# Optimization experiments

Measured on AMD Instinct MI355X. Metric: run time of the kernel, lower is better.

Reference implementation:

```python
import jax, jax.numpy as jnp
import numpy as np
from jax import lax

SELECTION_SIZE = 2  # top-k experts per token


def setup_inputs() -> dict:
    key = jax.random.key(0)
    k1, k2, k3, k4 = jax.random.split(key, 4)
    N, E, IN, OUT = 8192, 8, 2048, 2048
    X = jax.random.normal(k1, (N, IN), dtype=jnp.float32)
    G = jax.random.normal(k2, (N, E), dtype=jnp.float32)
    # expert Linear params: y = x @ W_e.T + b_e, W_e: [out, in]
    W = jax.random.normal(k3, (E, OUT, IN), dtype=jnp.float32) * (1.0 / np.sqrt(IN))
    b = jax.random.normal(k4, (E, OUT), dtype=jnp.float32) * 0.01
    return {"X": X, "G": G, "W": W, "b": b}


def reference(X, G, W, b):
    # softmax gating over experts, then top-k selection and renormalization
    raw_weights = jax.nn.softmax(G, axis=1)                      # [N, E]
    top_w, top_idx = lax.top_k(raw_weights, SELECTION_SIZE)      # [N, k]
    norm_w = top_w / jnp.sum(top_w, axis=1, keepdims=True)       # [N, k]

    # dense all-expert GEMM (same math as per-expert gathered matmuls)
    all_Y = jnp.einsum('ni,eoi->neo', X, W) + b[None, :, :]      # [N, E, out]

    # gather the top-k experts' outputs per token and combine
    sel_Y = jnp.take_along_axis(all_Y, top_idx[:, :, None], axis=1)  # [N, k, out]
    Y = jnp.einsum('nk,nko->no', norm_w, sel_Y)                  # [N, out]
    return Y
```

## Files before the change

kernel.cpp:

```cpp
#include <hip/hip_runtime.h>
#include <hip/hip_bf16.h>

#define N_TOK 8192
#define N_EXP 8
#define DIM_IN 2048
#define DIM_OUT 2048

#define BM 256
#define BN 256
#define BK 64
#define NKT (DIM_IN / BK)

#define NX_ELEMS (N_TOK * DIM_IN)
#define NW_ELEMS (N_EXP * DIM_OUT * DIM_IN)

typedef __attribute__((ext_vector_type(8))) short bf16x8_t;
typedef __attribute__((ext_vector_type(8))) short s16x8_t;
typedef __attribute__((ext_vector_type(4))) short s16x4_t;
typedef __attribute__((ext_vector_type(4))) float f32x4_t;

__device__ __forceinline__ short f2bf(float f) {
    union { __hip_bfloat16 h; short s; } u;
    u.h = __float2bfloat16(f);
    return u.s;
}

__device__ __forceinline__ void gload_lds16(const void* g, void* l) {
    __builtin_amdgcn_global_load_lds(
        (const __attribute__((address_space(1))) void*)g,
        (__attribute__((address_space(3))) void*)l, 16, 0, 0);
}

__global__ void moe_zero_kernel(float4* __restrict__ y, int n4, int* __restrict__ counts) {
    int i = blockIdx.x * blockDim.x + threadIdx.x;
    if (i < N_EXP) counts[i] = 0;
    float4 z; z.x = 0.f; z.y = 0.f; z.z = 0.f; z.w = 0.f;
    for (; i < n4; i += gridDim.x * blockDim.x) y[i] = z;
}

__global__ void moe_cvt_kernel(const float* __restrict__ X, const float* __restrict__ W,
                               unsigned short* __restrict__ Xb, unsigned short* __restrict__ Wb,
                               const int* __restrict__ counts, int* __restrict__ base) {
    if (blockIdx.x == 0 && threadIdx.x == 0) {
        int s = 0;
#pragma unroll
        for (int e = 0; e < N_EXP; ++e) { base[e] = s; s += counts[e]; }
        base[N_EXP] = s;
    }
    const long long total8 = (long long)(NX_ELEMS + NW_ELEMS) / 8;
    for (long long i = blockIdx.x * blockDim.x + threadIdx.x; i < total8;
         i += (long long)gridDim.x * blockDim.x) {
        long long b8 = i * 8;
        const float* src;
        unsigned short* dst;
        if (b8 < NX_ELEMS) { src = X + b8; dst = Xb + b8; }
        else { src = W + (b8 - NX_ELEMS); dst = Wb + (b8 - NX_ELEMS); }
        float4 a = *(const float4*)src;
        float4 b = *(const float4*)(src + 4);
        s16x8_t h;
        h[0] = f2bf(a.x); h[1] = f2bf(a.y); h[2] = f2bf(a.z); h[3] = f2bf(a.w);
        h[4] = f2bf(b.x); h[5] = f2bf(b.y); h[6] = f2bf(b.z); h[7] = f2bf(b.w);
        *(s16x8_t*)dst = h;
    }
}

__global__ void moe_gate_kernel(const float* __restrict__ G,
                                int* __restrict__ counts,
                                int* __restrict__ lists,
                                float* __restrict__ lw,
                                int* __restrict__ slotA, int* __restrict__ slotB,
                                float* __restrict__ wAo, float* __restrict__ wBo) {
    int t = blockIdx.x * blockDim.x + threadIdx.x;
    if (t >= N_TOK) return;
    float g[N_EXP];
#pragma unroll
    for (int e = 0; e < N_EXP; ++e) g[e] = G[t * N_EXP + e];
    int i0 = 0; float b0 = g[0];
#pragma unroll
    for (int e = 1; e < N_EXP; ++e) if (g[e] > b0) { b0 = g[e]; i0 = e; }
    int i1 = -1; float b1 = -INFINITY;
#pragma unroll
    for (int e = 0; e < N_EXP; ++e) if (e != i0 && g[e] > b1) { b1 = g[e]; i1 = e; }
    float e1 = expf(b1 - b0);
    float w0 = 1.0f / (1.0f + e1);
    float w1 = e1 * w0;
    int p0 = atomicAdd(&counts[i0], 1);
    lists[i0 * N_TOK + p0] = t;
    lw[i0 * N_TOK + p0] = w0;
    int p1 = atomicAdd(&counts[i1], 1);
    lists[i1 * N_TOK + p1] = t;
    lw[i1 * N_TOK + p1] = w1;
    slotA[t] = (i0 << 13) | p0;
    slotB[t] = (i1 << 13) | p1;
    wAo[t] = w0;
    wBo[t] = w1;
}

__global__ __launch_bounds__(256) void moe_combine_kernel(
        const float* __restrict__ scratch, const int* __restrict__ base,
        const int* __restrict__ slotA, const int* __restrict__ slotB,
        const float* __restrict__ wA, const float* __restrict__ wB,
        float* __restrict__ Y) {
    const int t = blockIdx.x;
    const int c = threadIdx.x * 8;
    const int sa = slotA[t];
    const int sb = slotB[t];
    const long gA = base[sa >> 13] + (sa & 8191);
    const long gB = base[sb >> 13] + (sb & 8191);
    const float wa = wA[t], wb = wB[t];
    const f32x4_t* ra = (const f32x4_t*)(scratch + gA * DIM_OUT + c);
    const f32x4_t* rb = (const f32x4_t*)(scratch + gB * DIM_OUT + c);
    f32x4_t* y = (f32x4_t*)(Y + (long)t * DIM_OUT + c);
#pragma unroll
    for (int i = 0; i < 2; ++i) {
        f32x4_t a = __builtin_nontemporal_load(ra + i);
        f32x4_t b = __builtin_nontemporal_load(rb + i);
        y[i] = wa * a + wb * b;
    }
}

__global__ __launch_bounds__(512, 2) void moe_gemm_bf16(
        const unsigned short* __restrict__ Xb, const unsigned short* __restrict__ Wb,
        const float* __restrict__ bias,
        const int* __restrict__ counts, const int* __restrict__ lists,
        const float* __restrict__ lw, const int* __restrict__ base,
        float* __restrict__ scratch, float* __restrict__ Y) {
    const int e = blockIdx.z;
    const int M = counts[e];
    const int m0 = blockIdx.y * BM;
    if (m0 >= M) return;
    const int col0 = blockIdx.x * BN;

    __shared__ unsigned short As[2][BM * BK];
    __shared__ unsigned short Bs[2][BN * BK];

    const int tid = threadIdx.x;
    const int lane = tid & 63;
    const int wid = tid >> 6;
    const int wm = (wid >> 2) * 128;
    const int wn = (wid & 3) * 64;

    const int* mylist = lists + e * N_TOK + m0;
    const float* lwp = lw + e * N_TOK + m0;

    const int srow = tid >> 3;
    const int scol = ((tid & 7) ^ (srow & 7)) * 8;

    const unsigned short* aptr[4];
#pragma unroll
    for (int i = 0; i < 4; ++i) {
        int r = srow + 64 * i;
        int tok = (m0 + r < M) ? mylist[r] : mylist[0];
        aptr[i] = Xb + (size_t)tok * DIM_IN + scol;
    }
    const unsigned short* bptr = Wb + ((size_t)e * DIM_OUT + col0 + srow) * DIM_IN + scol;

    const int ldsbase = wid * 512;

    const int rl = lane & 15;
    const int hi = lane >> 4;
    unsigned vA[2], vB[2];
#pragma unroll
    for (int kk = 0; kk < 2; ++kk) {
        unsigned x = (unsigned)(((kk << 6) | (hi << 4)) ^ ((rl & 7) << 4));
        vA[kk] = (unsigned)((wm + rl) * 128) + x;
        vB[kk] = (unsigned)((wn + rl) * 128) + x;
    }
    const char* AsC = (const char*)As;
    const char* BsC = (const char*)Bs;

    f32x4_t acc[8][4];
#pragma unroll
    for (int m = 0; m < 8; ++m)
#pragma unroll
        for (int n = 0; n < 4; ++n)
            acc[m][n] = (f32x4_t)(0.0f);

#define STAGE_A_H(buf, h, koff)                                                 \
    do {                                                                        \
        _Pragma("unroll")                                                       \
        for (int i = 2 * (h); i < 2 * (h) + 2; ++i)                             \
            gload_lds16(aptr[i] + (koff), &As[buf][i * 4096 + ldsbase]);        \
    } while (0)
#define STAGE_B_H(buf, h, koff)                                                 \
    do {                                                                        \
        _Pragma("unroll")                                                       \
        for (int i = 2 * (h); i < 2 * (h) + 2; ++i)                             \
            gload_lds16(bptr + (size_t)(i * 64) * DIM_IN + (koff),              \
                        &Bs[buf][i * 4096 + ldsbase]);                          \
    } while (0)

    STAGE_A_H(0, 0, 0);  STAGE_A_H(0, 1, 0);  STAGE_B_H(0, 0, 0);  STAGE_B_H(0, 1, 0);
    STAGE_A_H(1, 0, BK); STAGE_A_H(1, 1, BK); STAGE_B_H(1, 0, BK);

#define DO_TILE(CC, KOFN, KOF2)                                                 \
    {                                                                           \
        asm volatile("s_waitcnt vmcnt(6)" ::: "memory");                        \
        __builtin_amdgcn_s_barrier();                                           \
        asm volatile("" ::: "memory");                                          \
        STAGE_B_H(1 - (CC), 1, (KOFN));                                         \
        bf16x8_t bfr[4][2], af0[4][2], af1[4][2];                               \
        _Pragma("unroll")                                                       \
        for (int n = 0; n < 4; ++n)                                             \
            _Pragma("unroll")                                                   \
            for (int kk = 0; kk < 2; ++kk)                                      \
                bfr[n][kk] = *(const bf16x8_t*)(BsC + vB[kk] + ((CC) * 32768 + n * 2048)); \
        _Pragma("unroll")                                                       \
        for (int m = 0; m < 4; ++m)                                             \
            _Pragma("unroll")                                                   \
            for (int kk = 0; kk < 2; ++kk)                                      \
                af0[m][kk] = *(const bf16x8_t*)(AsC + vA[kk] + ((CC) * 32768 + m * 2048)); \
        __builtin_amdgcn_s_setprio(1);                                          \
        _Pragma("unroll")                                                       \
        for (int m = 0; m < 2; ++m)                                             \
            _Pragma("unroll")                                                   \
            for (int n = 0; n < 4; ++n)                                         \
                _Pragma("unroll")                                               \
                for (int kk = 0; kk < 2; ++kk)                                  \
                    acc[m][n] = __builtin_amdgcn_mfma_f32_16x16x32_bf16(af0[m][kk], bfr[n][kk], acc[m][n], 0, 0, 0); \
        __builtin_amdgcn_s_setprio(0);                                          \
        _Pragma("unroll")                                                       \
        for (int m = 0; m < 4; ++m)                                             \
            _Pragma("unroll")                                                   \
            for (int kk = 0; kk < 2; ++kk)                                      \
                af1[m][kk] = *(const bf16x8_t*)(AsC + vA[kk] + ((CC) * 32768 + (m + 4) * 2048)); \
        __builtin_amdgcn_s_setprio(1);                                          \
        _Pragma("unroll")                                                       \
        for (int m = 2; m < 4; ++m)                                             \
            _Pragma("unroll")                                                   \
            for (int n = 0; n < 4; ++n)                                         \
                _Pragma("unroll")                                               \
                for (int kk = 0; kk < 2; ++kk)                                  \
                    acc[m][n] = __builtin_amdgcn_mfma_f32_16x16x32_bf16(af0[m][kk], bfr[n][kk], acc[m][n], 0, 0, 0); \
        __builtin_amdgcn_s_setprio(0);                                          \
        asm volatile("s_waitcnt lgkmcnt(0)" ::: "memory");                      \
        __builtin_amdgcn_sched_barrier(0);                                      \
        __builtin_amdgcn_s_barrier();                                           \
        asm volatile("" ::: "memory");                                          \
        STAGE_A_H((CC), 0, (KOF2));                                             \
        __builtin_amdgcn_s_setprio(1);                                          \
        _Pragma("unroll")                                                       \
        for (int m = 0; m < 2; ++m)                                             \
            _Pragma("unroll")                                                   \
            for (int n = 0; n < 4; ++n)                                         \
                _Pragma("unroll")                                               \
                for (int kk = 0; kk < 2; ++kk)                                  \
                    acc[m + 4][n] = __builtin_amdgcn_mfma_f32_16x16x32_bf16(af1[m][kk], bfr[n][kk], acc[m + 4][n], 0, 0, 0); \
        __builtin_amdgcn_s_setprio(0);                                          \
        STAGE_A_H((CC), 1, (KOF2));                                             \
        __builtin_amdgcn_s_setprio(1);                                          \
        _Pragma("unroll")                                                       \
        for (int n = 0; n < 4; ++n)                                             \
            _Pragma("unroll")                                                   \
            for (int kk = 0; kk < 2; ++kk)                                      \
                acc[6][n] = __builtin_amdgcn_mfma_f32_16x16x32_bf16(af1[2][kk], bfr[n][kk], acc[6][n], 0, 0, 0); \
        __builtin_amdgcn_s_setprio(0);                                          \
        STAGE_B_H((CC), 0, (KOF2));                                             \
        __builtin_amdgcn_s_setprio(1);                                          \
        _Pragma("unroll")                                                       \
        for (int n = 0; n < 4; ++n)                                             \
            _Pragma("unroll")                                                   \
            for (int kk = 0; kk < 2; ++kk)                                      \
                acc[7][n] = __builtin_amdgcn_mfma_f32_16x16x32_bf16(af1[3][kk], bfr[n][kk], acc[7][n], 0, 0, 0); \
        __builtin_amdgcn_s_setprio(0);                                          \
    }

    for (int kt = 0; kt < NKT; kt += 2) {
        const int kofn0 = (kt + 1) * BK;
        const int kof20 = ((kt + 2 < NKT) ? (kt + 2) : (NKT - 1)) * BK;
        const int kofn1 = kof20;
        const int kof21 = ((kt + 3 < NKT) ? (kt + 3) : (NKT - 1)) * BK;
        DO_TILE(0, kofn0, kof20)
        DO_TILE(1, kofn1, kof21)
    }
    asm volatile("s_waitcnt vmcnt(0)" ::: "memory");
#undef DO_TILE
#undef STAGE_A_H
#undef STAGE_B_H

    const int cl = lane & 15;
    const int rq = (lane >> 4) << 2;
    float biasv[4];
#pragma unroll
    for (int n = 0; n < 4; ++n) biasv[n] = bias[e * DIM_OUT + col0 + wn + n * 16 + cl];

    if (scratch) {
        const int segbase = base[e] + m0;
#pragma unroll
        for (int m = 0; m < 8; ++m) {
#pragma unroll
            for (int j = 0; j < 4; ++j) {
                int row = wm + (m << 4) + rq + j;
                if (m0 + row < M) {
                    float* out = scratch + (size_t)(segbase + row) * DIM_OUT + col0 + wn;
#pragma unroll
                    for (int n = 0; n < 4; ++n)
                        __builtin_nontemporal_store(acc[m][n][j] + biasv[n], out + n * 16 + cl);
                }
            }
        }
    } else {
#pragma unroll
        for (int m = 0; m < 8; ++m) {
#pragma unroll
            for (int j = 0; j < 4; ++j) {
                int row = wm + (m << 4) + rq + j;
                if (m0 + row < M) {
                    int tok = mylist[row];
                    float wgt = lwp[row];
                    float* yrow = Y + (size_t)tok * DIM_OUT + col0 + wn;
#pragma unroll
                    for (int n = 0; n < 4; ++n)
                        atomicAdd(yrow + n * 16 + cl, wgt * (acc[m][n][j] + biasv[n]));
                }
            }
        }
    }
}

__global__ __launch_bounds__(256, 2) void moe_gemm_f32(
        const float* __restrict__ X, const float* __restrict__ W,
        const float* __restrict__ bias,
        const int* __restrict__ counts, const int* __restrict__ lists,
        const float* __restrict__ lw, float* __restrict__ Y) {
    const int e = blockIdx.z;
    const int M = counts[e];
    const int m0 = blockIdx.y * 128;
    if (m0 >= M) return;
    const int col0 = blockIdx.x * 128;

    __shared__ short As[128 * 64];
    __shared__ short Bs[128 * 64];
    char* Ab = (char*)As;
    char* Bb = (char*)Bs;

    const int tid = threadIdx.x;
    const int lane = tid & 63;
    const int wid = tid >> 6;
    const int wm = (wid >> 1) * 64;
    const int wn = (wid & 1) * 64;

    const int* mylist = lists + e * N_TOK + m0;
    const float* lwp = lw + e * N_TOK + m0;

    const int srow = tid >> 4;
    const int scol = (tid & 15) << 2;
    const int swzW = (srow & 7) << 4;

    const float* xptr[8];
#pragma unroll
    for (int p = 0; p < 8; ++p) {
        int r = p * 16 + srow;
        int tok = (m0 + r < M) ? mylist[r] : mylist[0];
        xptr[p] = X + (size_t)tok * DIM_IN + scol;
    }
    const float* wptr = W + ((size_t)e * DIM_OUT + col0 + srow) * DIM_IN + scol;

    f32x4_t acc[4][4];
#pragma unroll
    for (int m = 0; m < 4; ++m)
#pragma unroll
        for (int n = 0; n < 4; ++n)
            acc[m][n] = (f32x4_t)(0.0f);

    for (int k0 = 0; k0 < DIM_IN; k0 += 64) {
#pragma unroll
        for (int p = 0; p < 8; ++p) {
            int r = p * 16 + srow;
            unsigned byteoff = (unsigned)(r * 128 + scol * 2) ^ swzW;
            float4 va = *(const float4*)(xptr[p] + k0);
            s16x4_t ha; ha[0] = f2bf(va.x); ha[1] = f2bf(va.y); ha[2] = f2bf(va.z); ha[3] = f2bf(va.w);
            *(s16x4_t*)(Ab + byteoff) = ha;
            float4 vb = *(const float4*)(wptr + (size_t)p * 16 * DIM_IN + k0);
            s16x4_t hb; hb[0] = f2bf(vb.x); hb[1] = f2bf(vb.y); hb[2] = f2bf(vb.z); hb[3] = f2bf(vb.w);
            *(s16x4_t*)(Bb + byteoff) = hb;
        }
        __syncthreads();

#pragma unroll
        for (int kk = 0; kk < 2; ++kk) {
            const int kb = (kk << 6) + ((lane >> 4) << 4);
            bf16x8_t af[4], bfr[4];
#pragma unroll
            for (int m = 0; m < 4; ++m) {
                int r = wm + (m << 4) + (lane & 15);
                unsigned byteoff = (unsigned)(r * 128 + kb) ^ ((unsigned)(r & 7) << 4);
                af[m] = *(const bf16x8_t*)(Ab + byteoff);
            }
#pragma unroll
            for (int n = 0; n < 4; ++n) {
                int r = wn + (n << 4) + (lane & 15);
                unsigned byteoff = (unsigned)(r * 128 + kb) ^ ((unsigned)(r & 7) << 4);
                bfr[n] = *(const bf16x8_t*)(Bb + byteoff);
            }
#pragma unroll
            for (int m = 0; m < 4; ++m)
#pragma unroll
                for (int n = 0; n < 4; ++n)
                    acc[m][n] = __builtin_amdgcn_mfma_f32_16x16x32_bf16(af[m], bfr[n], acc[m][n], 0, 0, 0);
        }
        __syncthreads();
    }

    const int cl = lane & 15;
    const int rq = (lane >> 4) << 2;
    float biasv[4];
#pragma unroll
    for (int n = 0; n < 4; ++n) biasv[n] = bias[e * DIM_OUT + col0 + wn + n * 16 + cl];
#pragma unroll
    for (int m = 0; m < 4; ++m) {
#pragma unroll
        for (int j = 0; j < 4; ++j) {
            int row = wm + (m << 4) + rq + j;
            if (m0 + row < M) {
                int tok = mylist[row];
                float wgt = lwp[row];
                float* yrow = Y + (size_t)tok * DIM_OUT + col0 + wn;
#pragma unroll
                for (int n = 0; n < 4; ++n)
                    atomicAdd(yrow + n * 16 + cl, wgt * (acc[m][n][j] + biasv[n]));
            }
        }
    }
}

extern "C" void kernel_launch(void* const* d_in, const int* in_sizes, int n_in,
                              void* d_out, int out_size, void* d_ws, size_t ws_size,
                              hipStream_t stream) {
    const float* X = (const float*)d_in[0];
    const float* G = (const float*)d_in[1];
    const float* W = (const float*)d_in[2];
    const float* b = (const float*)d_in[3];
    float* Y = (float*)d_out;

    char* ws = (char*)d_ws;
    int*   counts = (int*)ws;
    int*   base   = (int*)(ws + 64);
    int*   slotA  = (int*)(ws + 256);
    int*   slotB  = (int*)(ws + 256 + 32768);
    float* wA     = (float*)(ws + 256 + 65536);
    float* wB     = (float*)(ws + 256 + 98304);
    int*   lists  = (int*)(ws + 256 + 131072);
    float* lw     = (float*)(ws + 256 + 131072 + 262144);
    size_t o_Xb   = 256 + 131072 + 2 * 262144;
    unsigned short* Xb = (unsigned short*)(ws + o_Xb);
    size_t o_Wb   = o_Xb + (size_t)NX_ELEMS * 2;
    unsigned short* Wb = (unsigned short*)(ws + o_Wb);
    size_t o_scr  = o_Wb + (size_t)NW_ELEMS * 2;
    float* scratch = (float*)(ws + o_scr);
    const size_t ws_need_mid  = o_scr;
    const size_t ws_need_full = o_scr + (size_t)2 * N_TOK * DIM_OUT * 4;

    const bool use_scratch = (ws_size >= ws_need_full);
    const bool use_bf16    = (ws_size >= ws_need_mid);

    if (use_scratch) {
        moe_zero_kernel<<<1, 256, 0, stream>>>((float4*)Y, 0, counts);
    } else {
        moe_zero_kernel<<<2048, 256, 0, stream>>>((float4*)Y, out_size / 4, counts);
    }
    moe_gate_kernel<<<(N_TOK + 255) / 256, 256, 0, stream>>>(G, counts, lists, lw,
                                                             slotA, slotB, wA, wB);

    if (use_bf16) {
        moe_cvt_kernel<<<2048, 256, 0, stream>>>(X, W, Xb, Wb, counts, base);
        dim3 grid(DIM_OUT / BN, N_TOK / BM, N_EXP);
        moe_gemm_bf16<<<grid, 512, 0, stream>>>(Xb, Wb, b, counts, lists, lw, base,
                                                use_scratch ? scratch : nullptr, Y);
        if (use_scratch) {
            moe_combine_kernel<<<N_TOK, 256, 0, stream>>>(scratch, base, slotA, slotB,
                                                          wA, wB, Y);
        }
    } else {
        dim3 grid(DIM_OUT / 128, N_TOK / 128, N_EXP);
        moe_gemm_f32<<<grid, 256, 0, stream>>>(X, W, b, counts, lists, lw, Y);
    }
}
```

Before: 328.8 us.

## Add half-height tail path for partial M tiles and nontemporal loads in convert

When an expert's last row tile holds at most 128 valid rows, the GEMM block now runs a separate path. That path loads and computes only 128 A rows, with 4x4 accumulators per warp instead of 8x4, which avoids MFMA and A-load work on padding rows. The full 256-row path is unchanged apart from moving into a branch. The fp32-to-bf16 convert kernel also switches to nontemporal vector loads. The cost is a larger kernel with two code paths, which may raise register or compile pressure and brings a different wait pattern in the tail loop.

```diff
diff --git a/kernel.cpp b/kernel.cpp
--- a/kernel.cpp
+++ b/kernel.cpp
@@ -55,11 +55,11 @@
         unsigned short* dst;
         if (b8 < NX_ELEMS) { src = X + b8; dst = Xb + b8; }
         else { src = W + (b8 - NX_ELEMS); dst = Wb + (b8 - NX_ELEMS); }
-        float4 a = *(const float4*)src;
-        float4 b = *(const float4*)(src + 4);
+        f32x4_t a = __builtin_nontemporal_load((const f32x4_t*)src);
+        f32x4_t b = __builtin_nontemporal_load((const f32x4_t*)(src + 4));
         s16x8_t h;
-        h[0] = f2bf(a.x); h[1] = f2bf(a.y); h[2] = f2bf(a.z); h[3] = f2bf(a.w);
-        h[4] = f2bf(b.x); h[5] = f2bf(b.y); h[6] = f2bf(b.z); h[7] = f2bf(b.w);
+        h[0] = f2bf(a[0]); h[1] = f2bf(a[1]); h[2] = f2bf(a[2]); h[3] = f2bf(a[3]);
+        h[4] = f2bf(b[0]); h[5] = f2bf(b[1]); h[6] = f2bf(b[2]); h[7] = f2bf(b[3]);
         *(s16x8_t*)dst = h;
     }
 }
@@ -129,6 +129,7 @@
     const int M = counts[e];
     const int m0 = blockIdx.y * BM;
     if (m0 >= M) return;
+    int vr = M - m0; if (vr > BM) vr = BM;
     const int col0 = blockIdx.x * BN;
 
     __shared__ unsigned short As[2][BM * BK];
@@ -137,7 +138,6 @@
     const int tid = threadIdx.x;
     const int lane = tid & 63;
     const int wid = tid >> 6;
-    const int wm = (wid >> 2) * 128;
     const int wn = (wid & 3) * 64;
 
     const int* mylist = lists + e * N_TOK + m0;
@@ -146,42 +146,15 @@
     const int srow = tid >> 3;
     const int scol = ((tid & 7) ^ (srow & 7)) * 8;
 
-    const unsigned short* aptr[4];
-#pragma unroll
-    for (int i = 0; i < 4; ++i) {
-        int r = srow + 64 * i;
-        int tok = (m0 + r < M) ? mylist[r] : mylist[0];
-        aptr[i] = Xb + (size_t)tok * DIM_IN + scol;
-    }
     const unsigned short* bptr = Wb + ((size_t)e * DIM_OUT + col0 + srow) * DIM_IN + scol;
 
     const int ldsbase = wid * 512;
 
     const int rl = lane & 15;
     const int hi = lane >> 4;
-    unsigned vA[2], vB[2];
-#pragma unroll
-    for (int kk = 0; kk < 2; ++kk) {
-        unsigned x = (unsigned)(((kk << 6) | (hi << 4)) ^ ((rl & 7) << 4));
-        vA[kk] = (unsigned)((wm + rl) * 128) + x;
-        vB[kk] = (unsigned)((wn + rl) * 128) + x;
-    }
     const char* AsC = (const char*)As;
     const char* BsC = (const char*)Bs;
 
-    f32x4_t acc[8][4];
-#pragma unroll
-    for (int m = 0; m < 8; ++m)
-#pragma unroll
-        for (int n = 0; n < 4; ++n)
-            acc[m][n] = (f32x4_t)(0.0f);
-
-#define STAGE_A_H(buf, h, koff)                                                 \
-    do {                                                                        \
-        _Pragma("unroll")                                                       \
-        for (int i = 2 * (h); i < 2 * (h) + 2; ++i)                             \
-            gload_lds16(aptr[i] + (koff), &As[buf][i * 4096 + ldsbase]);        \
-    } while (0)
 #define STAGE_B_H(buf, h, koff)                                                 \
     do {                                                                        \
         _Pragma("unroll")                                                       \
@@ -190,8 +163,41 @@
                         &Bs[buf][i * 4096 + ldsbase]);                          \
     } while (0)
 
-    STAGE_A_H(0, 0, 0);  STAGE_A_H(0, 1, 0);  STAGE_B_H(0, 0, 0);  STAGE_B_H(0, 1, 0);
-    STAGE_A_H(1, 0, BK); STAGE_A_H(1, 1, BK); STAGE_B_H(1, 0, BK);
+    if (vr > 128) {
+        const int wm = (wid >> 2) * 128;
+
+        const unsigned short* aptr[4];
+#pragma unroll
+        for (int i = 0; i < 4; ++i) {
+            int r = srow + 64 * i;
+            int tok = (m0 + r < M) ? mylist[r] : mylist[0];
+            aptr[i] = Xb + (size_t)tok * DIM_IN + scol;
+        }
+
+        unsigned vA[2], vB[2];
+#pragma unroll
+        for (int kk = 0; kk < 2; ++kk) {
+            unsigned x = (unsigned)(((kk << 6) | (hi << 4)) ^ ((rl & 7) << 4));
+            vA[kk] = (unsigned)((wm + rl) * 128) + x;
+            vB[kk] = (unsigned)((wn + rl) * 128) + x;
+        }
+
+        f32x4_t acc[8][4];
+#pragma unroll
+        for (int m = 0; m < 8; ++m)
+#pragma unroll
+            for (int n = 0; n < 4; ++n)
+                acc[m][n] = (f32x4_t)(0.0f);
+
+#define STAGE_A_H(buf, h, koff)                                                 \
+    do {                                                                        \
+        _Pragma("unroll")                                                       \
+        for (int i = 2 * (h); i < 2 * (h) + 2; ++i)                             \
+            gload_lds16(aptr[i] + (koff), &As[buf][i * 4096 + ldsbase]);        \
+    } while (0)
+
+        STAGE_A_H(0, 0, 0);  STAGE_A_H(0, 1, 0);  STAGE_B_H(0, 0, 0);  STAGE_B_H(0, 1, 0);
+        STAGE_A_H(1, 0, BK); STAGE_A_H(1, 1, BK); STAGE_B_H(1, 0, BK);
 
 #define DO_TILE(CC, KOFN, KOF2)                                                 \
     {                                                                           \
@@ -265,57 +271,187 @@
         __builtin_amdgcn_s_setprio(0);                                          \
     }
 
-    for (int kt = 0; kt < NKT; kt += 2) {
-        const int kofn0 = (kt + 1) * BK;
-        const int kof20 = ((kt + 2 < NKT) ? (kt + 2) : (NKT - 1)) * BK;
-        const int kofn1 = kof20;
-        const int kof21 = ((kt + 3 < NKT) ? (kt + 3) : (NKT - 1)) * BK;
-        DO_TILE(0, kofn0, kof20)
-        DO_TILE(1, kofn1, kof21)
-    }
-    asm volatile("s_waitcnt vmcnt(0)" ::: "memory");
-#undef DO_TILE
-#undef STAGE_A_H
-#undef STAGE_B_H
-
-    const int cl = lane & 15;
-    const int rq = (lane >> 4) << 2;
-    float biasv[4];
-#pragma unroll
-    for (int n = 0; n < 4; ++n) biasv[n] = bias[e * DIM_OUT + col0 + wn + n * 16 + cl];
-
-    if (scratch) {
-        const int segbase = base[e] + m0;
-#pragma unroll
-        for (int m = 0; m < 8; ++m) {
-#pragma unroll
-            for (int j = 0; j < 4; ++j) {
-                int row = wm + (m << 4) + rq + j;
-                if (m0 + row < M) {
-                    float* out = scratch + (size_t)(segbase + row) * DIM_OUT + col0 + wn;
-#pragma unroll
-                    for (int n = 0; n < 4; ++n)
-                        __builtin_nontemporal_store(acc[m][n][j] + biasv[n], out + n * 16 + cl);
+        for (int kt = 0; kt < NKT; kt += 2) {
+            const int kofn0 = (kt + 1) * BK;
+            const int kof20 = ((kt + 2 < NKT) ? (kt + 2) : (NKT - 1)) * BK;
+            const int kofn1 = kof20;
+            const int kof21 = ((kt + 3 < NKT) ? (kt + 3) : (NKT - 1)) * BK;
+            DO_TILE(0, kofn0, kof20)
+            DO_TILE(1, kofn1, kof21)
+        }
+        asm volatile("s_waitcnt vmcnt(0)" ::: "memory");
+
+        const int cl = lane & 15;
+        const int rq = (lane >> 4) << 2;
+        float biasv[4];
+#pragma unroll
+        for (int n = 0; n < 4; ++n) biasv[n] = bias[e * DIM_OUT + col0 + wn + n * 16 + cl];
+
+        if (scratch) {
+            const int segbase = base[e] + m0;
+#pragma unroll
+            for (int m = 0; m < 8; ++m) {
+#pragma unroll
+                for (int j = 0; j < 4; ++j) {
+                    int row = wm + (m << 4) + rq + j;
+                    if (m0 + row < M) {
+                        float* out = scratch + (size_t)(segbase + row) * DIM_OUT + col0 + wn;
+#pragma unroll
+                        for (int n = 0; n < 4; ++n)
+                            __builtin_nontemporal_store(acc[m][n][j] + biasv[n], out + n * 16 + cl);
+                    }
                 }
             }
-        }
-    } else {
-#pragma unroll
-        for (int m = 0; m < 8; ++m) {
-#pragma unroll
-            for (int j = 0; j < 4; ++j) {
-                int row = wm + (m << 4) + rq + j;
-                if (m0 + row < M) {
-                    int tok = mylist[row];
-                    float wgt = lwp[row];
-                    float* yrow = Y + (size_t)tok * DIM_OUT + col0 + wn;
-#pragma unroll
-                    for (int n = 0; n < 4; ++n)
-                        atomicAdd(yrow + n * 16 + cl, wgt * (acc[m][n][j] + biasv[n]));
+        } else {
+#pragma unroll
+            for (int m = 0; m < 8; ++m) {
+#pragma unroll
+                for (int j = 0; j < 4; ++j) {
+                    int row = wm + (m << 4) + rq + j;
+                    if (m0 + row < M) {
+                        int tok = mylist[row];
+                        float wgt = lwp[row];
+                        float* yrow = Y + (size_t)tok * DIM_OUT + col0 + wn;
+#pragma unroll
+                        for (int n = 0; n < 4; ++n)
+                            atomicAdd(yrow + n * 16 + cl, wgt * (acc[m][n][j] + biasv[n]));
+                    }
                 }
             }
         }
-    }
+    } else {
+        const int wm = (wid >> 2) * 64;
+
+        const unsigned short* aptrT[2];
+#pragma unroll
+        for (int i = 0; i < 2; ++i) {
+            int r = srow + 64 * i;
+            int tok = (m0 + r < M) ? mylist[r] : mylist[0];
+            aptrT[i] = Xb + (size_t)tok * DIM_IN + scol;
+        }
+
+        unsigned vA[2], vB[2];
+#pragma unroll
+        for (int kk = 0; kk < 2; ++kk) {
+            unsigned x = (unsigned)(((kk << 6) | (hi << 4)) ^ ((rl & 7) << 4));
+            vA[kk] = (unsigned)((wm + rl) * 128) + x;
+            vB[kk] = (unsigned)((wn + rl) * 128) + x;
+        }
+
+        f32x4_t acc[4][4];
+#pragma unroll
+        for (int m = 0; m < 4; ++m)
+#pragma unroll
+            for (int n = 0; n < 4; ++n)
+                acc[m][n] = (f32x4_t)(0.0f);
+
+#define STAGE_A_T(buf, koff)                                                    \
+    do {                                                                        \
+        _Pragma("unroll")                                                       \
+        for (int i = 0; i < 2; ++i)                                             \
+            gload_lds16(aptrT[i] + (koff), &As[buf][i * 4096 + ldsbase]);       \
+    } while (0)
+
+        STAGE_A_T(0, 0);  STAGE_B_H(0, 0, 0);  STAGE_B_H(0, 1, 0);
+        STAGE_A_T(1, BK); STAGE_B_H(1, 0, BK);
+
+#define DO_TILE_T(CC, KOFN, KOF2)                                               \
+    {                                                                           \
+        asm volatile("s_waitcnt vmcnt(4)" ::: "memory");                        \
+        __builtin_amdgcn_s_barrier();                                           \
+        asm volatile("" ::: "memory");                                          \
+        STAGE_B_H(1 - (CC), 1, (KOFN));                                         \
+        bf16x8_t bfr[4][2], af[4][2];                                           \
+        _Pragma("unroll")                                                       \
+        for (int n = 0; n < 4; ++n)                                             \
+            _Pragma("unroll")                                                   \
+            for (int kk = 0; kk < 2; ++kk)                                      \
+                bfr[n][kk] = *(const bf16x8_t*)(BsC + vB[kk] + ((CC) * 32768 + n * 2048)); \
+        _Pragma("unroll")                                                       \
+        for (int m = 0; m < 4; ++m)                                             \
+            _Pragma("unroll")                                                   \
+            for (int kk = 0; kk < 2; ++kk)                                      \
+                af[m][kk] = *(const bf16x8_t*)(AsC + vA[kk] + ((CC) * 32768 + m * 2048)); \
+        __builtin_amdgcn_s_setprio(1);                                          \
+        _Pragma("unroll")                                                       \
+        for (int m = 0; m < 2; ++m)                                             \
+            _Pragma("unroll")                                                   \
+            for (int n = 0; n < 4; ++n)                                         \
+                _Pragma("unroll")                                               \
+                for (int kk = 0; kk < 2; ++kk)                                  \
+                    acc[m][n] = __builtin_amdgcn_mfma_f32_16x16x32_bf16(af[m][kk], bfr[n][kk], acc[m][n], 0, 0, 0); \
+        __builtin_amdgcn_s_setprio(0);                                          \
+        asm volatile("s_waitcnt lgkmcnt(0)" ::: "memory");                      \
+        __builtin_amdgcn_sched_barrier(0);                                      \
+        __builtin_amdgcn_s_barrier();                                           \
+        asm volatile("" ::: "memory");                                          \
+        STAGE_A_T((CC), (KOF2));                                                \
+        __builtin_amdgcn_s_setprio(1);                                          \
+        _Pragma("unroll")                                                       \
+        for (int m = 2; m < 4; ++m)                                             \
+            _Pragma("unroll")                                                   \
+            for (int n = 0; n < 4; ++n)                                         \
+                _Pragma("unroll")                                               \
+                for (int kk = 0; kk < 2; ++kk)                                  \
+                    acc[m][n] = __builtin_amdgcn_mfma_f32_16x16x32_bf16(af[m][kk], bfr[n][kk], acc[m][n], 0, 0, 0); \
+        __builtin_amdgcn_s_setprio(0);                                          \
+        STAGE_B_H((CC), 0, (KOF2));                                             \
+    }
+
+        for (int kt = 0; kt < NKT; kt += 2) {
+            const int kofn0 = (kt + 1) * BK;
+            const int kof20 = ((kt + 2 < NKT) ? (kt + 2) : (NKT - 1)) * BK;
+            const int kofn1 = kof20;
+            const int kof21 = ((kt + 3 < NKT) ? (kt + 3) : (NKT - 1)) * BK;
+            DO_TILE_T(0, kofn0, kof20)
+            DO_TILE_T(1, kofn1, kof21)
+        }
+        asm volatile("s_waitcnt vmcnt(0)" ::: "memory");
+
+        const int cl = lane & 15;
+        const int rq = (lane >> 4) << 2;
+        float biasv[4];
+#pragma unroll
+        for (int n = 0; n < 4; ++n) biasv[n] = bias[e * DIM_OUT + col0 + wn + n * 16 + cl];
+
+        if (scratch) {
+            const int segbase = base[e] + m0;
+#pragma unroll
+            for (int m = 0; m < 4; ++m) {
+#pragma unroll
+                for (int j = 0; j < 4; ++j) {
+                    int row = wm + (m << 4) + rq + j;
+                    if (m0 + row < M) {
+                        float* out = scratch + (size_t)(segbase + row) * DIM_OUT + col0 + wn;
+#pragma unroll
+                        for (int n = 0; n < 4; ++n)
+                            __builtin_nontemporal_store(acc[m][n][j] + biasv[n], out + n * 16 + cl);
+                    }
+                }
+            }
+        } else {
+#pragma unroll
+            for (int m = 0; m < 4; ++m) {
+#pragma unroll
+                for (int j = 0; j < 4; ++j) {
+                    int row = wm + (m << 4) + rq + j;
+                    if (m0 + row < M) {
+                        int tok = mylist[row];
+                        float wgt = lwp[row];
+                        float* yrow = Y + (size_t)tok * DIM_OUT + col0 + wn;
+#pragma unroll
+                        for (int n = 0; n < 4; ++n)
+                            atomicAdd(yrow + n * 16 + cl, wgt * (acc[m][n][j] + biasv[n]));
+                    }
+                }
+            }
+        }
+    }
+#undef DO_TILE
+#undef DO_TILE_T
+#undef STAGE_A_H
+#undef STAGE_A_T
+#undef STAGE_B_H
 }
 
 __global__ __launch_bounds__(256, 2) void moe_gemm_f32(
```

Result: no change. 332.8 us (+1.2%).
